# Kernel optimization log

Measured on AMD Instinct MI355X. Metric: run time of the kernel, lower is better.

Reference implementation:

```python
import jax, jax.numpy as jnp
import numpy as np
from jax import lax


def setup_inputs() -> dict:
    key = jax.random.key(0)
    k1, k2, k3, k4 = jax.random.split(key, 4)
    B, C_in, H, W = 16, 64, 256, 256
    E, C_out, KH, KW = 4, 64, 3, 3
    inputs = jax.random.normal(k1, (B, C_in, H, W), dtype=jnp.float32)
    weight = jax.random.normal(k2, (E, C_out, C_in, KH, KW), dtype=jnp.float32) * 0.05
    fc_w = jax.random.normal(k3, (E, C_in), dtype=jnp.float32) * 0.1
    fc_b = jax.random.normal(k4, (E,), dtype=jnp.float32) * 0.1
    return {
        "inputs": inputs,
        "weight": weight,
        "fc_w": fc_w,
        "fc_b": fc_b,
        "stride": 1,
        "dilation": 1,
        "padding": 1,
    }


def reference(inputs, weight, fc_w, fc_b, stride, dilation, padding):
    # inputs: [B, C_in, H, W]; weight: [E, C_out, C_in, KH, KW]
    # Routing: adaptive avg pool to 1x1 == spatial mean, then Linear -> sigmoid.
    # (Dropout is identity in eval mode.)
    pooled = jnp.mean(inputs, axis=(2, 3))                      # [B, C_in]
    routing = jax.nn.sigmoid(pooled @ fc_w.T + fc_b)            # [B, E]
    # Per-sample mixed kernels.
    kernels = jnp.einsum("be,eoikl->boikl", routing, weight)    # [B, C_out, C_in, KH, KW]

    def conv_one(x, k):
        # x: [C_in, H, W], k: [C_out, C_in, KH, KW]
        y = lax.conv_general_dilated(
            x[None],
            k,
            window_strides=(stride, stride),
            padding=[(padding, padding), (padding, padding)],
            rhs_dilation=(dilation, dilation),
            dimension_numbers=("NCHW", "OIHW", "NCHW"),
        )
        return y[0]

    return jax.vmap(conv_one)(inputs, kernels)                  # [B, C_out, H', W']
```

## Files before the change

### kernel.cpp

```cpp
#include <hip/hip_runtime.h>
#include <math.h>

#define B_   16
#define CIN  64
#define COUT 64
#define H_   256
#define W_   256

typedef short s16x8  __attribute__((ext_vector_type(8)));
typedef float f32x16 __attribute__((ext_vector_type(16)));

__device__ __forceinline__ void split_bf16(float v, unsigned short& hi, unsigned short& lo) {
    unsigned u = __float_as_uint(v);
    hi = (unsigned short)(u >> 16);
    float hif = __uint_as_float(u & 0xffff0000u);
    lo = (unsigned short)(__float_as_uint(v - hif) >> 16);
}

__global__ __launch_bounds__(256) void pool_kernel(const float* __restrict__ x,
                                                   float* __restrict__ pooled) {
    const int plane = blockIdx.x;
    const float4* p = (const float4*)(x + (size_t)plane * (H_ * W_));
    float s = 0.f;
    for (int i = threadIdx.x; i < (H_ * W_) / 4; i += 256) {
        float4 v = p[i];
        s += (v.x + v.y) + (v.z + v.w);
    }
    #pragma unroll
    for (int off = 32; off > 0; off >>= 1) s += __shfl_down(s, off);
    __shared__ float red[4];
    if ((threadIdx.x & 63) == 0) red[threadIdx.x >> 6] = s;
    __syncthreads();
    if (threadIdx.x == 0)
        pooled[plane] = (red[0] + red[1] + red[2] + red[3]) * (1.f / (H_ * W_));
}

__global__ void routing_kernel(const float* __restrict__ pooled,
                               const float* __restrict__ fc_w,
                               const float* __restrict__ fc_b,
                               float* __restrict__ routing) {
    const int tid = threadIdx.x;
    const int b = tid >> 2, e = tid & 3;
    float s = fc_b[e];
    for (int c = 0; c < CIN; ++c) s += pooled[b * CIN + c] * fc_w[e * CIN + c];
    routing[b * 4 + e] = 1.f / (1.f + expf(-s));
}

__global__ __launch_bounds__(256) void mix_kernel(const float* __restrict__ routing,
                                                  const float* __restrict__ weight,
                                                  unsigned short* __restrict__ mixed) {
    const int gid = blockIdx.x * 256 + threadIdx.x;
    const int icL = gid & 15;
    const int oc  = (gid >> 4) & 63;
    const int q   = (gid >> 10) & 3;
    const int b   = gid >> 12;
    const int ic  = q * 16 + icL;

    float r[4];
    #pragma unroll
    for (int e = 0; e < 4; ++e) r[e] = routing[b * 4 + e];

    float s[9];
    #pragma unroll
    for (int t = 0; t < 9; ++t) s[t] = 0.f;
    #pragma unroll
    for (int e = 0; e < 4; ++e) {
        const float* wp = weight + (((size_t)e * COUT + oc) * CIN + ic) * 9;
        #pragma unroll
        for (int t = 0; t < 9; ++t) s[t] = fmaf(r[e], wp[t], s[t]);
    }
    unsigned short* base = mixed + (size_t)(b * 4 + q) * 18432;
    const int mb = oc >> 5;
    const int l  = (oc & 31) + ((icL >> 3) << 5);
    const int j  = icL & 7;
    #pragma unroll
    for (int t = 0; t < 9; ++t) {
        unsigned short hi, lo;
        split_bf16(s[t], hi, lo);
        base[(t * 4 + 0 + mb) * 512 + l * 8 + j] = hi;
        base[(t * 4 + 2 + mb) * 512 + l * 8 + j] = lo;
    }
}

__global__ __launch_bounds__(256, 2) void conv_kernel(const float* __restrict__ x,
                                                      const unsigned short* __restrict__ wmix,
                                                      float* __restrict__ y) {
    __shared__ __align__(16) unsigned short in_s[4 * 340 * 8];

    const int tid  = threadIdx.x;
    const int lane = tid & 63;
    const int wv   = tid >> 6;
    const int n    = lane & 31;
    const int kseg = lane >> 5;

    const int bid = blockIdx.x;
    const int wg  = (bid & 7) * 512 + (bid >> 3);
    const int w0 = (wg & 7) * 32;
    const int h0 = ((wg >> 3) & 31) * 8;
    const int b  = wg >> 8;

    const int p0 = tid;
    const int r0 = p0 / 34, c0 = p0 - r0 * 34;
    const int p1 = tid + 256;
    const int r1 = p1 / 34, c1 = p1 - r1 * 34;
    const bool has1 = (p1 < 340);

    const int gh0 = h0 - 1 + r0, gw0 = w0 - 1 + c0;
    const int gh1 = h0 - 1 + r1, gw1 = w0 - 1 + c1;
    const bool ok0 = ((unsigned)gh0 < H_) && ((unsigned)gw0 < W_);
    const bool ok1 = has1 && ((unsigned)gh1 < H_) && ((unsigned)gw1 < W_);

    const float* xb = x + (size_t)b * CIN * H_ * W_;
    const float* g0 = xb + (ok0 ? (gh0 * W_ + gw0) : 0);
    const float* g1 = xb + (ok1 ? (gh1 * W_ + gw1) : 0);

    #define LOAD16(dst, gp, okf, qq) do {                                   \
        const float* _p = (gp) + (size_t)(qq) * 16 * (H_ * W_);             \
        _Pragma("unroll")                                                   \
        for (int _i = 0; _i < 16; ++_i)                                     \
            dst[_i] = (okf) ? _p[(size_t)_i * (H_ * W_)] : 0.f;             \
    } while (0)

    #define STAGE(pp, regs) do {                                            \
        s16x8 _h0, _h1, _l0, _l1;                                           \
        _Pragma("unroll")                                                   \
        for (int _i = 0; _i < 8; ++_i) {                                    \
            unsigned short _h, _l;                                          \
            split_bf16(regs[_i], _h, _l);                                   \
            _h0[_i] = (short)_h; _l0[_i] = (short)_l;                       \
            split_bf16(regs[8 + _i], _h, _l);                               \
            _h1[_i] = (short)_h; _l1[_i] = (short)_l;                       \
        }                                                                   \
        ((s16x8*)in_s)[0 * 340 + (pp)] = _h0;                               \
        ((s16x8*)in_s)[1 * 340 + (pp)] = _h1;                               \
        ((s16x8*)in_s)[2 * 340 + (pp)] = _l0;                               \
        ((s16x8*)in_s)[3 * 340 + (pp)] = _l1;                               \
    } while (0)

    f32x16 acc[2][2];
    #pragma unroll
    for (int mb = 0; mb < 2; ++mb)
        #pragma unroll
        for (int nb = 0; nb < 2; ++nb)
            #pragma unroll
            for (int j = 0; j < 16; ++j) acc[mb][nb][j] = 0.f;

    const unsigned short* wb = wmix + (size_t)b * 4 * 18432 + lane * 8;

    #pragma unroll 1
    for (int q = 0; q < 4; ++q) {
        __syncthreads();
        {
            float xr[16];
            LOAD16(xr, g0, ok0, q);
            STAGE(p0, xr);
            if (has1) { LOAD16(xr, g1, ok1, q); STAGE(p1, xr); }
        }
        __syncthreads();
        const unsigned short* wq = wb + q * 18432;

        #pragma unroll
        for (int kw = 0; kw < 3; ++kw) {
            s16x8 aH[3][2], aL[3][2];
            #pragma unroll
            for (int kh = 0; kh < 3; ++kh) {
                const int tap = kh * 3 + kw;
                #pragma unroll
                for (int mb = 0; mb < 2; ++mb) {
                    aH[kh][mb] = *(const s16x8*)(wq + (tap * 4 + 0 + mb) * 512);
                    aL[kh][mb] = *(const s16x8*)(wq + (tap * 4 + 2 + mb) * 512);
                }
            }
            s16x8 bh[4], bl[4];
            #pragma unroll
            for (int r = 0; r < 4; ++r) {
                const int pos = (wv * 2 + r) * 34 + n + kw;
                bh[r] = ((const s16x8*)in_s)[(0 + kseg) * 340 + pos];
                bl[r] = ((const s16x8*)in_s)[(2 + kseg) * 340 + pos];
            }
            #pragma unroll
            for (int kh = 0; kh < 3; ++kh) {
                #pragma unroll
                for (int nb = 0; nb < 2; ++nb) {
                    const int r = nb + kh;
                    #pragma unroll
                    for (int mb = 0; mb < 2; ++mb) {
                        acc[mb][nb] = __builtin_amdgcn_mfma_f32_32x32x16_bf16(aH[kh][mb], bh[r], acc[mb][nb], 0, 0, 0);
                        acc[mb][nb] = __builtin_amdgcn_mfma_f32_32x32x16_bf16(aL[kh][mb], bh[r], acc[mb][nb], 0, 0, 0);
                        acc[mb][nb] = __builtin_amdgcn_mfma_f32_32x32x16_bf16(aH[kh][mb], bl[r], acc[mb][nb], 0, 0, 0);
                    }
                }
            }
        }
    }

    #pragma unroll
    for (int mb = 0; mb < 2; ++mb) {
        #pragma unroll
        for (int nb = 0; nb < 2; ++nb) {
            const int hrow = h0 + wv * 2 + nb;
            #pragma unroll
            for (int r = 0; r < 16; ++r) {
                const int oc = mb * 32 + (r & 3) + 8 * (r >> 2) + 4 * kseg;
                y[(((size_t)b * COUT + oc) * H_ + hrow) * W_ + w0 + n] = acc[mb][nb][r];
            }
        }
    }
}

extern "C" void kernel_launch(void* const* d_in, const int* in_sizes, int n_in,
                              void* d_out, int out_size, void* d_ws, size_t ws_size,
                              hipStream_t stream) {
    const float* x      = (const float*)d_in[0];
    const float* weight = (const float*)d_in[1];
    const float* fc_w   = (const float*)d_in[2];
    const float* fc_b   = (const float*)d_in[3];
    float* out = (float*)d_out;

    float* ws      = (float*)d_ws;
    float* pooled  = ws;
    float* routing = ws + 1024;
    unsigned short* mixed = (unsigned short*)(ws + 1088);

    pool_kernel<<<B_ * CIN, 256, 0, stream>>>(x, pooled);
    routing_kernel<<<1, 64, 0, stream>>>(pooled, fc_w, fc_b, routing);
    mix_kernel<<<(B_ * 4 * COUT * 16) / 256, 256, 0, stream>>>(routing, weight, mixed);

    conv_kernel<<<4096, 256, 0, stream>>>(x, mixed, out);
}
```

Measured before the change: 640.2 us.

## Double-buffer input tile in LDS and prefetch next channel group into registers

The input tile staging buffer in LDS is doubled. Global loads for the next 16-channel group are issued into registers before the MFMA work on the current group, then split to bf16 and written to the other buffer afterwards. This overlaps global memory latency with compute and drops one barrier per iteration. The cost is twice the LDS (about 43 KB per block) and 16 more live float registers per thread, which may hurt occupancy at the launch bound of 2 blocks.

```diff
diff --git a/kernel.cpp b/kernel.cpp
--- a/kernel.cpp
+++ b/kernel.cpp
@@ -85,7 +85,7 @@
 __global__ __launch_bounds__(256, 2) void conv_kernel(const float* __restrict__ x,
                                                       const unsigned short* __restrict__ wmix,
                                                       float* __restrict__ y) {
-    __shared__ __align__(16) unsigned short in_s[4 * 340 * 8];
+    __shared__ __align__(16) unsigned short in_s[2 * 4 * 340 * 8];
 
     const int tid  = threadIdx.x;
     const int lane = tid & 63;
@@ -121,7 +121,7 @@
             dst[_i] = (okf) ? _p[(size_t)_i * (H_ * W_)] : 0.f;             \
     } while (0)
 
-    #define STAGE(pp, regs) do {                                            \
+    #define STAGE(bb, pp, regs) do {                                        \
         s16x8 _h0, _h1, _l0, _l1;                                           \
         _Pragma("unroll")                                                   \
         for (int _i = 0; _i < 8; ++_i) {                                    \
@@ -131,10 +131,10 @@
             split_bf16(regs[8 + _i], _h, _l);                               \
             _h1[_i] = (short)_h; _l1[_i] = (short)_l;                       \
         }                                                                   \
-        ((s16x8*)in_s)[0 * 340 + (pp)] = _h0;                               \
-        ((s16x8*)in_s)[1 * 340 + (pp)] = _h1;                               \
-        ((s16x8*)in_s)[2 * 340 + (pp)] = _l0;                               \
-        ((s16x8*)in_s)[3 * 340 + (pp)] = _l1;                               \
+        ((s16x8*)in_s)[(bb) * 1360 + 0 * 340 + (pp)] = _h0;                 \
+        ((s16x8*)in_s)[(bb) * 1360 + 1 * 340 + (pp)] = _h1;                 \
+        ((s16x8*)in_s)[(bb) * 1360 + 2 * 340 + (pp)] = _l0;                 \
+        ((s16x8*)in_s)[(bb) * 1360 + 3 * 340 + (pp)] = _l1;                 \
     } while (0)
 
     f32x16 acc[2][2];
@@ -146,18 +146,24 @@
             for (int j = 0; j < 16; ++j) acc[mb][nb][j] = 0.f;
 
     const unsigned short* wb = wmix + (size_t)b * 4 * 18432 + lane * 8;
+
+    float xr0[16], xr1[16];
+
+    LOAD16(xr0, g0, ok0, 0);
+    if (has1) LOAD16(xr1, g1, ok1, 0);
+    STAGE(0, p0, xr0);
+    if (has1) STAGE(0, p1, xr1);
+    __syncthreads();
 
     #pragma unroll 1
     for (int q = 0; q < 4; ++q) {
-        __syncthreads();
-        {
-            float xr[16];
-            LOAD16(xr, g0, ok0, q);
-            STAGE(p0, xr);
-            if (has1) { LOAD16(xr, g1, ok1, q); STAGE(p1, xr); }
-        }
-        __syncthreads();
+        const int cur = q & 1;
+        if (q < 3) {
+            LOAD16(xr0, g0, ok0, q + 1);
+            if (has1) LOAD16(xr1, g1, ok1, q + 1);
+        }
         const unsigned short* wq = wb + q * 18432;
+        const s16x8* bs = (const s16x8*)in_s + cur * 1360;
 
         #pragma unroll
         for (int kw = 0; kw < 3; ++kw) {
@@ -175,8 +181,8 @@
             #pragma unroll
             for (int r = 0; r < 4; ++r) {
                 const int pos = (wv * 2 + r) * 34 + n + kw;
-                bh[r] = ((const s16x8*)in_s)[(0 + kseg) * 340 + pos];
-                bl[r] = ((const s16x8*)in_s)[(2 + kseg) * 340 + pos];
+                bh[r] = bs[(0 + kseg) * 340 + pos];
+                bl[r] = bs[(2 + kseg) * 340 + pos];
             }
             #pragma unroll
             for (int kh = 0; kh < 3; ++kh) {
@@ -192,6 +198,12 @@
                 }
             }
         }
+
+        if (q < 3) {
+            STAGE(cur ^ 1, p0, xr0);
+            if (has1) STAGE(cur ^ 1, p1, xr1);
+            __syncthreads();
+        }
     }
 
     #pragma unroll
```

Measured after the change: 661.4 us. 3.3% more time.
